# Performance work log

Hardware: AMD Instinct MI355X
Metric: run time of the kernel (lower is better)

Reference implementation:

```python
import jax, jax.numpy as jnp
import numpy as np

VOCAB = 50257
BATCH = 512
SEQ = 1024


def setup_inputs() -> dict:
    key = jax.random.key(0)
    kx, kidf = jax.random.split(key)
    x = jax.random.randint(kx, (BATCH, SEQ), 0, VOCAB, dtype=jnp.int64)
    # idf weights are positive; uniform in (0.1, 5.0) mimics real idf values
    idf = jax.random.uniform(kidf, (VOCAB,), dtype=jnp.float32, minval=0.1, maxval=5.0)
    return {"x": x, "idf": idf}


def reference(x, idf):
    B, S = x.shape
    V = idf.shape[0]
    # term-frequency histogram: scatter-add directly into (B, V) accumulator,
    # equivalent to the one-hot scatter_ + sum over seq in the original
    rows = jnp.arange(B, dtype=x.dtype)[:, None]           # (B, 1)
    tf = jnp.zeros((B, V), dtype=jnp.float32).at[rows, x].add(1.0)
    tfidf = tf * idf                                        # (B, V)
    n = jnp.sum(tfidf, axis=1, keepdims=True)               # (B, 1)
    return tfidf / n
```

## Files before the change

### kernel.cpp

```cpp
#include <hip/hip_runtime.h>


constexpr int VOCAB  = 50257;
constexpr int SEQ    = 1024;
constexpr int BATCH  = 512;
constexpr int NSEG   = 4;
constexpr int SEGLEN = (VOCAB + NSEG - 1) / NSEG;
constexpr int NT     = 256;

__global__ __launch_bounds__(NT)
void tfidf_kernel(const int* __restrict__ x,
                  const float* __restrict__ idf,
                  float* __restrict__ out) {
    __shared__ float seg[SEGLEN];
    __shared__ float red[NT / 64];

    const int blk = blockIdx.x;
    const int b   = blk >> 2;
    const int s   = blk & 3;
    const int tid = threadIdx.x;

    const int lo  = s * SEGLEN;
    const int len = (SEGLEN < VOCAB - lo) ? SEGLEN : (VOCAB - lo);

    const int4 t4 = ((const int4*)(x + (size_t)b * SEQ))[tid];

    {
        float4* z = (float4*)seg;
        const float4 z4 = make_float4(0.f, 0.f, 0.f, 0.f);
        for (int c = tid; c < SEGLEN / 4; c += NT) z[c] = z4;
        if (tid < SEGLEN - (SEGLEN / 4) * 4) seg[(SEGLEN / 4) * 4 + tid] = 0.f;
    }

    const float i0 = idf[t4.x], i1 = idf[t4.y], i2 = idf[t4.z], i3 = idf[t4.w];
    float v = (i0 + i1) + (i2 + i3);
    #pragma unroll
    for (int off = 32; off > 0; off >>= 1) v += __shfl_down(v, off, 64);
    if ((tid & 63) == 0) red[tid >> 6] = v;
    __syncthreads();
    const float inv_n = 1.0f / ((red[0] + red[1]) + (red[2] + red[3]));

    if (t4.x >= lo && t4.x < lo + len) atomicAdd(&seg[t4.x - lo], i0 * inv_n);
    if (t4.y >= lo && t4.y < lo + len) atomicAdd(&seg[t4.y - lo], i1 * inv_n);
    if (t4.z >= lo && t4.z < lo + len) atomicAdd(&seg[t4.z - lo], i2 * inv_n);
    if (t4.w >= lo && t4.w < lo + len) atomicAdd(&seg[t4.w - lo], i3 * inv_n);
    __syncthreads();

    const size_t g0 = (size_t)b * VOCAB + lo;
    float* __restrict__ o = out + g0;
    const int head = (int)((4 - (g0 & 3)) & 3);
    const int n4   = (len - head) >> 2;
    const int tail = len - head - (n4 << 2);

    if (tid < head) o[tid] = seg[tid];
    float4* __restrict__ p4 = (float4*)(o + head);
    for (int c = tid; c < n4; c += NT) {
        const int i = head + (c << 2);
        p4[c] = make_float4(seg[i], seg[i + 1], seg[i + 2], seg[i + 3]);
    }
    if (tid < tail) {
        const int i = head + (n4 << 2) + tid;
        o[i] = seg[i];
    }
}

extern "C" void kernel_launch(void* const* d_in, const int* in_sizes, int n_in,
                              void* d_out, int out_size, void* d_ws, size_t ws_size,
                              hipStream_t stream) {
    const int*   x   = (const int*)d_in[0];
    const float* idf = (const float*)d_in[1];
    float*       out = (float*)d_out;
    tfidf_kernel<<<dim3(BATCH * NSEG), dim3(NT), 0, stream>>>(x, idf, out);
}
```

Before: 114.2 us.

## Split TF-IDF into histogram-compaction pass and sparse scatter-write pass

The single kernel is replaced with two passes when enough workspace is available. Pass 1 builds one full-vocabulary 16-bit packed count histogram per row in LDS, then compacts the nonzero entries into per-segment lists in global workspace. Pass 2 zero-fills 8K-element segments, scatters the sparse entries and streams them out with float4 stores. This removes the repeated per-segment token filtering of the old kernel, at the cost of an extra launch and a workspace round trip. The old kernel is kept as a fallback when workspace is too small.

Result: slower. 133.4 us (+16.8%).

```diff
diff --git a/kernel.cpp b/kernel.cpp
--- a/kernel.cpp
+++ b/kernel.cpp
@@ -1,37 +1,152 @@
 #include <hip/hip_runtime.h>
 
 
-constexpr int VOCAB  = 50257;
-constexpr int SEQ    = 1024;
-constexpr int BATCH  = 512;
-constexpr int NSEG   = 4;
-constexpr int SEGLEN = (VOCAB + NSEG - 1) / NSEG;
-constexpr int NT     = 256;
+constexpr int VOCAB = 50257;
+constexpr int SEQ   = 1024;
+constexpr int BATCH = 512;
 
-__global__ __launch_bounds__(NT)
-void tfidf_kernel(const int* __restrict__ x,
-                  const float* __restrict__ idf,
-                  float* __restrict__ out) {
-    __shared__ float seg[SEGLEN];
-    __shared__ float red[NT / 64];
+constexpr int HWORDS   = (VOCAB + 1) / 2;
+constexpr int HWORDS4  = ((HWORDS + 3) / 4) * 4;
+constexpr int NTA      = 1024;
+constexpr int SEGSHIFT = 13;
+constexpr int SEGLEN   = 1 << SEGSHIFT;
+constexpr int NSEG     = (VOCAB + SEGLEN - 1) / SEGLEN;
+constexpr int MAXNZ    = 1024;
+constexpr size_t COUNTS_BYTES = 16384;
+
+__global__ __launch_bounds__(NTA)
+void tfidf_pass1(const int* __restrict__ x, const float* __restrict__ idf,
+                 int* __restrict__ counts, int2* __restrict__ entries) {
+    __shared__ __align__(16) unsigned int cnt[HWORDS4];
+    __shared__ float red[NTA / 64];
+    __shared__ int nzc[NSEG];
+
+    const int b   = blockIdx.x;
+    const int tid = threadIdx.x;
+
+    {
+        uint4* z = (uint4*)cnt;
+        const uint4 z4 = make_uint4(0u, 0u, 0u, 0u);
+        for (int i = tid; i < HWORDS4 / 4; i += NTA) z[i] = z4;
+    }
+    if (tid < NSEG) nzc[tid] = 0;
+    __syncthreads();
+
+    const int tok = x[(size_t)b * SEQ + tid];
+    const float my_idf = idf[tok];
+    atomicAdd(&cnt[tok >> 1], (tok & 1) ? 65536u : 1u);
+
+    float v = my_idf;
+    #pragma unroll
+    for (int off = 32; off > 0; off >>= 1) v += __shfl_down(v, off, 64);
+    if ((tid & 63) == 0) red[tid >> 6] = v;
+    __syncthreads();
+
+    float nsum = 0.0f;
+    #pragma unroll
+    for (int w = 0; w < NTA / 64; ++w) nsum += red[w];
+    const float inv_n = 1.0f / nsum;
+
+    for (int w4 = tid; w4 < HWORDS4 / 4; w4 += NTA) {
+        const uint4 u4 = ((const uint4*)cnt)[w4];
+        const unsigned uu[4] = {u4.x, u4.y, u4.z, u4.w};
+        #pragma unroll
+        for (int j = 0; j < 4; ++j) {
+            const unsigned u = uu[j];
+            if (u == 0u) continue;
+            const int id0 = (w4 * 4 + j) * 2;
+            const unsigned c0 = u & 0xffffu;
+            const unsigned c1 = u >> 16;
+            if (c0) {
+                const int seg = id0 >> SEGSHIFT;
+                const int pos = atomicAdd(&nzc[seg], 1);
+                entries[((size_t)b * NSEG + seg) * MAXNZ + pos] =
+                    make_int2(id0, __float_as_int((float)c0 * idf[id0] * inv_n));
+            }
+            if (c1) {
+                const int id1 = id0 + 1;
+                const int seg = id1 >> SEGSHIFT;
+                const int pos = atomicAdd(&nzc[seg], 1);
+                entries[((size_t)b * NSEG + seg) * MAXNZ + pos] =
+                    make_int2(id1, __float_as_int((float)c1 * idf[id1] * inv_n));
+            }
+        }
+    }
+    __syncthreads();
+    if (tid < NSEG) counts[b * NSEG + tid] = nzc[tid];
+}
+
+__global__ __launch_bounds__(256)
+void tfidf_pass2(const int* __restrict__ counts, const int2* __restrict__ entries,
+                 float* __restrict__ out) {
+    __shared__ __align__(16) float seg[SEGLEN];
+
+    const int bi  = blockIdx.x;
+    const int b   = bi / NSEG;
+    const int s   = bi - b * NSEG;
+    const int tid = threadIdx.x;
+
+    const int n = counts[b * NSEG + s];
+    const int2* __restrict__ e = entries + ((size_t)b * NSEG + s) * MAXNZ;
+
+    {
+        float4* z = (float4*)seg;
+        const float4 z4 = make_float4(0.f, 0.f, 0.f, 0.f);
+        for (int c = tid; c < SEGLEN / 4; c += 256) z[c] = z4;
+    }
+    __syncthreads();
+
+    for (int i = tid; i < n; i += 256) {
+        const int2 p = e[i];
+        seg[p.x & (SEGLEN - 1)] = __int_as_float(p.y);
+    }
+    __syncthreads();
+
+    const int lo  = s << SEGSHIFT;
+    const int len = (SEGLEN < VOCAB - lo) ? SEGLEN : (VOCAB - lo);
+    const size_t g0 = (size_t)b * VOCAB + lo;
+    float* __restrict__ o = out + g0;
+
+    const int head = (int)((4 - (g0 & 3)) & 3);
+    const int n4   = (len - head) >> 2;
+    const int tail = len - head - (n4 << 2);
+
+    if (tid < head) o[tid] = seg[tid];
+    float4* __restrict__ p4 = (float4*)(o + head);
+    for (int c = tid; c < n4; c += 256) {
+        const int i = head + (c << 2);
+        p4[c] = make_float4(seg[i], seg[i + 1], seg[i + 2], seg[i + 3]);
+    }
+    if (tid < tail) {
+        const int i = head + (n4 << 2) + tid;
+        o[i] = seg[i];
+    }
+}
+
+constexpr int FSEG    = 4;
+constexpr int FSEGLEN = (VOCAB + FSEG - 1) / FSEG;
+
+__global__ __launch_bounds__(256)
+void tfidf_fallback(const int* __restrict__ x, const float* __restrict__ idf,
+                    float* __restrict__ out) {
+    __shared__ float seg[FSEGLEN];
+    __shared__ float red[4];
 
     const int blk = blockIdx.x;
     const int b   = blk >> 2;
     const int s   = blk & 3;
     const int tid = threadIdx.x;
 
-    const int lo  = s * SEGLEN;
-    const int len = (SEGLEN < VOCAB - lo) ? SEGLEN : (VOCAB - lo);
+    const int lo  = s * FSEGLEN;
+    const int len = (FSEGLEN < VOCAB - lo) ? FSEGLEN : (VOCAB - lo);
 
     const int4 t4 = ((const int4*)(x + (size_t)b * SEQ))[tid];
-
     {
         float4* z = (float4*)seg;
         const float4 z4 = make_float4(0.f, 0.f, 0.f, 0.f);
-        for (int c = tid; c < SEGLEN / 4; c += NT) z[c] = z4;
-        if (tid < SEGLEN - (SEGLEN / 4) * 4) seg[(SEGLEN / 4) * 4 + tid] = 0.f;
+        for (int c = tid; c < FSEGLEN / 4; c += 256) z[c] = z4;
+        if (tid < FSEGLEN - (FSEGLEN / 4) * 4) seg[(FSEGLEN / 4) * 4 + tid] = 0.f;
     }
-
     const float i0 = idf[t4.x], i1 = idf[t4.y], i2 = idf[t4.z], i3 = idf[t4.w];
     float v = (i0 + i1) + (i2 + i3);
     #pragma unroll
@@ -54,7 +169,7 @@
 
     if (tid < head) o[tid] = seg[tid];
     float4* __restrict__ p4 = (float4*)(o + head);
-    for (int c = tid; c < n4; c += NT) {
+    for (int c = tid; c < n4; c += 256) {
         const int i = head + (c << 2);
         p4[c] = make_float4(seg[i], seg[i + 1], seg[i + 2], seg[i + 3]);
     }
@@ -70,5 +185,14 @@
     const int*   x   = (const int*)d_in[0];
     const float* idf = (const float*)d_in[1];
     float*       out = (float*)d_out;
-    tfidf_kernel<<<dim3(BATCH * NSEG), dim3(NT), 0, stream>>>(x, idf, out);
+
+    const size_t need = COUNTS_BYTES + (size_t)BATCH * NSEG * MAXNZ * sizeof(int2);
+    if (ws_size >= need) {
+        int*  counts  = (int*)d_ws;
+        int2* entries = (int2*)((char*)d_ws + COUNTS_BYTES);
+        tfidf_pass1<<<dim3(BATCH), dim3(NTA), 0, stream>>>(x, idf, counts, entries);
+        tfidf_pass2<<<dim3(BATCH * NSEG), dim3(256), 0, stream>>>(counts, entries, out);
+    } else {
+        tfidf_fallback<<<dim3(BATCH * FSEG), dim3(256), 0, stream>>>(x, idf, out);
+    }
 }
```

## Split normalizer into separate kernel and use integer count histogram with smaller segments

Applied to the files above, without the earlier changes.

Computes the per-row normalizer in a separate small kernel and writes it to workspace, then builds an integer count histogram in shared memory over 8192-entry vocab segments (7 segments instead of 4). The idf slice is staged in shared memory and the output is computed as count*idf*inv_n. This gives smaller per-block shared memory, which may allow more blocks per CU, and replaces float atomics with integer atomics. In exchange it adds a second launch and more blocks, each of which rereads the row of x.

After: 126.5 us. 10.8% more time.

```diff
diff --git a/kernel.cpp b/kernel.cpp
--- a/kernel.cpp
+++ b/kernel.cpp
@@ -1,49 +1,70 @@
 #include <hip/hip_runtime.h>
 
 
-constexpr int VOCAB  = 50257;
-constexpr int SEQ    = 1024;
-constexpr int BATCH  = 512;
-constexpr int NSEG   = 4;
-constexpr int SEGLEN = (VOCAB + NSEG - 1) / NSEG;
-constexpr int NT     = 256;
+constexpr int VOCAB = 50257;
+constexpr int SEQ   = 1024;
+constexpr int BATCH = 512;
+
+constexpr int SEGSHIFT = 13;
+constexpr int SEGLEN   = 1 << SEGSHIFT;
+constexpr int NSEG     = (VOCAB + SEGLEN - 1) / SEGLEN;
+constexpr int NT       = 256;
 
 __global__ __launch_bounds__(NT)
-void tfidf_kernel(const int* __restrict__ x,
-                  const float* __restrict__ idf,
-                  float* __restrict__ out) {
-    __shared__ float seg[SEGLEN];
+void inv_n_kernel(const int* __restrict__ x, const float* __restrict__ idf,
+                  float* __restrict__ inv_n) {
     __shared__ float red[NT / 64];
-
-    const int blk = blockIdx.x;
-    const int b   = blk >> 2;
-    const int s   = blk & 3;
+    const int b   = blockIdx.x;
     const int tid = threadIdx.x;
 
-    const int lo  = s * SEGLEN;
-    const int len = (SEGLEN < VOCAB - lo) ? SEGLEN : (VOCAB - lo);
-
     const int4 t4 = ((const int4*)(x + (size_t)b * SEQ))[tid];
-
-    {
-        float4* z = (float4*)seg;
-        const float4 z4 = make_float4(0.f, 0.f, 0.f, 0.f);
-        for (int c = tid; c < SEGLEN / 4; c += NT) z[c] = z4;
-        if (tid < SEGLEN - (SEGLEN / 4) * 4) seg[(SEGLEN / 4) * 4 + tid] = 0.f;
-    }
-
-    const float i0 = idf[t4.x], i1 = idf[t4.y], i2 = idf[t4.z], i3 = idf[t4.w];
-    float v = (i0 + i1) + (i2 + i3);
+    float v = (idf[t4.x] + idf[t4.y]) + (idf[t4.z] + idf[t4.w]);
     #pragma unroll
     for (int off = 32; off > 0; off >>= 1) v += __shfl_down(v, off, 64);
     if ((tid & 63) == 0) red[tid >> 6] = v;
     __syncthreads();
-    const float inv_n = 1.0f / ((red[0] + red[1]) + (red[2] + red[3]));
+    if (tid == 0)
+        inv_n[b] = 1.0f / ((red[0] + red[1]) + (red[2] + red[3]));
+}
 
-    if (t4.x >= lo && t4.x < lo + len) atomicAdd(&seg[t4.x - lo], i0 * inv_n);
-    if (t4.y >= lo && t4.y < lo + len) atomicAdd(&seg[t4.y - lo], i1 * inv_n);
-    if (t4.z >= lo && t4.z < lo + len) atomicAdd(&seg[t4.z - lo], i2 * inv_n);
-    if (t4.w >= lo && t4.w < lo + len) atomicAdd(&seg[t4.w - lo], i3 * inv_n);
+__global__ __launch_bounds__(NT)
+void tfidf_seg(const int* __restrict__ x, const float* __restrict__ idf,
+               const float* __restrict__ inv_n_arr, float* __restrict__ out) {
+    __shared__ __align__(16) unsigned int cnt[SEGLEN];
+    __shared__ __align__(16) float idf_s[SEGLEN];
+
+    const int bi  = blockIdx.x;
+    const int s   = bi >> 9;
+    const int b   = bi & (BATCH - 1);
+    const int tid = threadIdx.x;
+
+    const int lo  = s << SEGSHIFT;
+    const int len = (SEGLEN < VOCAB - lo) ? SEGLEN : (VOCAB - lo);
+
+    const int4  t4   = ((const int4*)(x + (size_t)b * SEQ))[tid];
+    const float rinv = inv_n_arr[b];
+
+    {
+        uint4* z = (uint4*)cnt;
+        const uint4 z4 = make_uint4(0u, 0u, 0u, 0u);
+        for (int c = tid; c < SEGLEN / 4; c += NT) z[c] = z4;
+    }
+    {
+        const float4* src = (const float4*)(idf + lo);
+        float4* dst = (float4*)idf_s;
+        for (int c = tid; c < (len >> 2); c += NT) dst[c] = src[c];
+        if (tid < (len & 3)) idf_s[(len & ~3) + tid] = idf[lo + (len & ~3) + tid];
+    }
+    __syncthreads();
+
+    {
+        const unsigned ul = (unsigned)len;
+        unsigned t;
+        t = (unsigned)(t4.x - lo); if (t < ul) atomicAdd(&cnt[t], 1u);
+        t = (unsigned)(t4.y - lo); if (t < ul) atomicAdd(&cnt[t], 1u);
+        t = (unsigned)(t4.z - lo); if (t < ul) atomicAdd(&cnt[t], 1u);
+        t = (unsigned)(t4.w - lo); if (t < ul) atomicAdd(&cnt[t], 1u);
+    }
     __syncthreads();
 
     const size_t g0 = (size_t)b * VOCAB + lo;
@@ -52,15 +73,18 @@
     const int n4   = (len - head) >> 2;
     const int tail = len - head - (n4 << 2);
 
-    if (tid < head) o[tid] = seg[tid];
+    if (tid < head) o[tid] = (float)cnt[tid] * idf_s[tid] * rinv;
     float4* __restrict__ p4 = (float4*)(o + head);
     for (int c = tid; c < n4; c += NT) {
         const int i = head + (c << 2);
-        p4[c] = make_float4(seg[i], seg[i + 1], seg[i + 2], seg[i + 3]);
+        p4[c] = make_float4((float)cnt[i]     * idf_s[i]     * rinv,
+                            (float)cnt[i + 1] * idf_s[i + 1] * rinv,
+                            (float)cnt[i + 2] * idf_s[i + 2] * rinv,
+                            (float)cnt[i + 3] * idf_s[i + 3] * rinv);
     }
     if (tid < tail) {
         const int i = head + (n4 << 2) + tid;
-        o[i] = seg[i];
+        o[i] = (float)cnt[i] * idf_s[i] * rinv;
     }
 }
 
@@ -70,5 +94,8 @@
     const int*   x   = (const int*)d_in[0];
     const float* idf = (const float*)d_in[1];
     float*       out = (float*)d_out;
-    tfidf_kernel<<<dim3(BATCH * NSEG), dim3(NT), 0, stream>>>(x, idf, out);
+    float*       inv_n = (float*)d_ws;
+
+    inv_n_kernel<<<dim3(BATCH), dim3(NT), 0, stream>>>(x, idf, inv_n);
+    tfidf_seg<<<dim3(BATCH * NSEG), dim3(NT), 0, stream>>>(x, idf, inv_n, out);
 }
```
